# Kernel tuning notes

Measured on AMD Instinct MI355X. Metric: run time of the kernel, lower is better.

The kernel has to match this reference:

```python
import jax, jax.numpy as jnp
import numpy as np

EPS = 1e-5

def rmsnorm(x, g):
    var = jnp.mean(jnp.square(x), axis=-1, keepdims=True)
    return x * jax.lax.rsqrt(var + EPS) * g

def setup_inputs() -> dict:
    key = jax.random.key(0)
    ks = jax.random.split(key, 8)
    B, S, T, D = 2, 2048, 2048, 1024
    H, HKV, HD = 16, 4, 64
    std = 0.02
    return {
        "x": jax.random.normal(ks[0], (B, S, D), jnp.float32),
        "kv": jax.random.normal(ks[1], (B, T, D), jnp.float32),
        "wq": jax.random.normal(ks[2], (H * HD, D), jnp.float32) * std,
        "wk": jax.random.normal(ks[3], (HKV * HD, D), jnp.float32) * std,
        "wv": jax.random.normal(ks[4], (HKV * HD, D), jnp.float32) * std,
        "wo": jax.random.normal(ks[5], (D, H * HD), jnp.float32) * std,
        "gq": jnp.ones((D,), jnp.float32),
        "gkv": jnp.ones((D,), jnp.float32),
    }

def reference(x, kv, wq, wk, wv, wo, gq, gkv):
    B, S, D = x.shape
    T = kv.shape[1]
    H, HKV, HD = 16, 4, 64
    R = H // HKV  # heads per kv group
    xn = rmsnorm(x, gq)
    kvn = rmsnorm(kv, gkv)
    # projections
    q = (xn @ wq.T).reshape(B, S, HKV, R, HD)   # grouped query heads
    k = (kvn @ wk.T).reshape(B, T, HKV, HD)
    v = (kvn @ wv.T).reshape(B, T, HKV, HD)
    scale = 1.0 / jnp.sqrt(jnp.float32(HD))
    # block-mask is None -> full dense cross attention; GQA via broadcast einsum
    scores = jnp.einsum('bsgrd,btgd->bgrst', q, k) * scale  # [B,HKV,R,S,T]
    probs = jax.nn.softmax(scores, axis=-1)
    out = jnp.einsum('bgrst,btgd->bsgrd', probs, v)  # [B,S,HKV,R,HD]
    out = out.reshape(B, S, H * HD) @ wo.T
    return x + out
```

## Files before the change

### kernel.cpp

```cpp
#include <hip/hip_runtime.h>

#define DEV __device__ __forceinline__

typedef __attribute__((ext_vector_type(8))) _Float16 h8;
typedef __attribute__((ext_vector_type(4))) float f32x4;
typedef __attribute__((ext_vector_type(16))) float f32x16;
typedef __fp16 __attribute__((ext_vector_type(2))) hh2;

DEV unsigned short f2h(float f) {
  union { _Float16 h[2]; unsigned short u[2]; } v;
  v.h[0] = (_Float16)f;
  return v.u[0];
}

DEV float h2f(unsigned short u) {
  union { _Float16 h[2]; unsigned short u[2]; } v;
  v.u[0] = u;
  return (float)v.h[0];
}

DEV void async_load16(const void* g, void* l) {
  __builtin_amdgcn_global_load_lds(
      (const __attribute__((address_space(1))) void*)g,
      (__attribute__((address_space(3))) void*)l,
      16, 0, 0);
}

DEV void pl32swap(unsigned int& a, unsigned int& b) {
  asm("v_permlane32_swap_b32 %0, %1" : "+v"(a), "+v"(b));
}


__global__ __launch_bounds__(256) void prep(const float* __restrict__ x,
                                            const float* __restrict__ kv,
                                            const float* __restrict__ wq,
                                            const float* __restrict__ wk,
                                            const float* __restrict__ wv,
                                            const float* __restrict__ wo,
                                            const float* __restrict__ gq,
                                            const float* __restrict__ gkv,
                                            unsigned short* __restrict__ wqb,
                                            unsigned short* __restrict__ wkvb,
                                            unsigned short* __restrict__ wob,
                                            unsigned short* __restrict__ xn,
                                            unsigned short* __restrict__ kvn,
                                            float qscale) {
  const int b = blockIdx.x, tid = threadIdx.x;
  if (b < 2560) {
    const float* src;
    unsigned short* dst;
    float sc = 1.0f;
    int base;
    if (b < 1024) { src = wq; dst = wqb; sc = qscale; base = b; }
    else if (b < 1280) { src = wk; dst = wkvb; base = b - 1024; }
    else if (b < 1536) { src = wv; dst = wkvb + 262144; base = b - 1280; }
    else { src = wo; dst = wob; base = b - 1536; }
    const int i = (base * 256 + tid) * 4;
    float4 v = *(const float4*)&src[i];
    ushort4 o;
    o.x = f2h(v.x * sc); o.y = f2h(v.y * sc);
    o.z = f2h(v.z * sc); o.w = f2h(v.w * sc);
    *(ushort4*)&dst[i] = o;
    return;
  }
  int row = b - 2560;
  const float* src;
  const float* g;
  unsigned short* dst;
  if (row < 4096) { src = x; g = gq; dst = xn; }
  else { row -= 4096; src = kv; g = gkv; dst = kvn; }
  const float* xr = src + (size_t)row * 1024;
  float4 v = *(const float4*)&xr[tid * 4];
  float ss = v.x * v.x + v.y * v.y + v.z * v.z + v.w * v.w;
  ss += __shfl_xor(ss, 32); ss += __shfl_xor(ss, 16);
  ss += __shfl_xor(ss, 8);  ss += __shfl_xor(ss, 4);
  ss += __shfl_xor(ss, 2);  ss += __shfl_xor(ss, 1);
  __shared__ float red[4];
  if ((tid & 63) == 0) red[tid >> 6] = ss;
  __syncthreads();
  float tot = red[0] + red[1] + red[2] + red[3];
  float inv = rsqrtf(tot * (1.0f / 1024.0f) + 1e-5f);
  float4 gv = *(const float4*)&g[tid * 4];
  ushort4 o;
  o.x = f2h(v.x * inv * gv.x); o.y = f2h(v.y * inv * gv.y);
  o.z = f2h(v.z * inv * gv.z); o.w = f2h(v.w * inv * gv.w);
  *(ushort4*)&dst[(size_t)row * 1024 + tid * 4] = o;
}

__global__ __launch_bounds__(256) void proj_gemm(const unsigned short* __restrict__ xn,
                                                 const unsigned short* __restrict__ kvn,
                                                 const unsigned short* __restrict__ wqb,
                                                 const unsigned short* __restrict__ wkvb,
                                                 unsigned short* __restrict__ qb,
                                                 unsigned short* __restrict__ kb,
                                                 unsigned short* __restrict__ vTb) {
  __shared__ unsigned short Al[2][2][128 * 32];
  __shared__ unsigned short Bl[2][2][64 * 32];
  const int tid = threadIdx.x;
  const int w = tid >> 6, l = tid & 63;
  const int quad = l >> 4, ln = l & 15;
  const int wm0 = (w >> 1) * 64, wn0 = (w & 1) * 32;
  const int r4 = l >> 2;
  const int c4s = (((l & 3) ^ ((l >> 3) & 3))) * 8;
  const int qs8 = (quad ^ ((l >> 1) & 3)) * 8;

  int z = blockIdx.x;
  const unsigned short *A, *W;
  int m0, n0, isq;
  if (z < 512) {
    A = xn; W = wqb; isq = 1;
    m0 = (((z >> 7) << 3) + (z & 7)) * 128;
    n0 = ((z >> 3) & 15) * 64;
  } else {
    z -= 512; A = kvn; W = wkvb; isq = 0;
    m0 = (((z >> 6) << 3) + (z & 7)) * 128;
    n0 = ((z >> 3) & 7) * 64;
  }

  f32x4 acc[4][2] = {};

  auto stage = [&](int buf, int kk) {
#pragma unroll
    for (int j = 0; j < 6; ++j) {
      const int idx = w * 6 + j;
      if (idx < 16) {
        const int p = idx >> 3, rb = (idx & 7) * 16;
        async_load16(A + (size_t)(m0 + rb + r4) * 1024 + kk + p * 32 + c4s,
                     &Al[buf][p][rb * 32]);
      } else {
        const int ib = idx - 16;
        const int p = ib >> 2, rb = (ib & 3) * 16;
        async_load16(W + (size_t)(n0 + rb + r4) * 1024 + kk + p * 32 + c4s,
                     &Bl[buf][p][rb * 32]);
      }
    }
  };

  stage(0, 0);
#pragma unroll 2
  for (int it = 0; it < 16; ++it) {
    const int buf = it & 1;
    __syncthreads();
    if (it < 15) stage(buf ^ 1, (it + 1) * 64);
#pragma unroll
    for (int kc = 0; kc < 2; ++kc) {
      h8 af[4], bf[2];
#pragma unroll
      for (int mi = 0; mi < 4; ++mi)
        af[mi] = *(const h8*)&Al[buf][kc][(wm0 + mi * 16 + ln) * 32 + qs8];
#pragma unroll
      for (int ni = 0; ni < 2; ++ni)
        bf[ni] = *(const h8*)&Bl[buf][kc][(wn0 + ni * 16 + ln) * 32 + qs8];
#pragma unroll
      for (int mi = 0; mi < 4; ++mi)
#pragma unroll
        for (int ni = 0; ni < 2; ++ni)
          acc[mi][ni] = __builtin_amdgcn_mfma_f32_16x16x32_f16(af[mi], bf[ni], acc[mi][ni], 0, 0, 0);
    }
  }

#pragma unroll
  for (int mi = 0; mi < 4; ++mi)
#pragma unroll
    for (int ni = 0; ni < 2; ++ni)
#pragma unroll
      for (int r = 0; r < 4; ++r) {
        const int row = m0 + wm0 + mi * 16 + quad * 4 + r;
        const int col = n0 + wn0 + ni * 16 + ln;
        const unsigned short v = f2h(acc[mi][ni][r]);
        if (isq) {
          qb[((size_t)row << 10) + col] = v;
        } else if (col < 256) {
          kb[(size_t)row * 256 + col] = v;
        } else {
          const int c2 = col - 256, gg = c2 >> 6, dd = c2 & 63;
          const int bb = row >> 11, t = row & 2047;
          vTb[((size_t)((bb * 4 + gg) * 64 + dd) << 11) + t] = v;
        }
      }
}

__global__ __launch_bounds__(256) void o_gemm(const unsigned short* __restrict__ O0,
                                              const unsigned short* __restrict__ O1,
                                              const float* __restrict__ l0p,
                                              const float* __restrict__ l1p,
                                              const unsigned short* __restrict__ wob,
                                              const float* __restrict__ x,
                                              float* __restrict__ out) {
  __shared__ unsigned short Al[2][2][128 * 32];
  __shared__ unsigned short Bl[2][2][64 * 32];
  __shared__ float Linv[16 * 128];
  const int tid = threadIdx.x;
  const int w = tid >> 6, l = tid & 63;
  const int quad = l >> 4, ln = l & 15;
  const int wm0 = (w >> 1) * 64, wn0 = (w & 1) * 32;
  const int r4 = l >> 2;
  const int c4s = (((l & 3) ^ ((l >> 3) & 3))) * 8;
  const int qs8 = (quad ^ ((l >> 1) & 3)) * 8;

  const int z = blockIdx.x;
  const int m0 = (((z >> 7) << 3) + (z & 7)) * 128;
  const int n0 = ((z >> 3) & 15) * 64;

  {
    const int h = tid >> 4, r0 = (tid & 15) * 8;
#pragma unroll
    for (int i = 0; i < 8; ++i) {
      const int r = r0 + i;
      const size_t li = (size_t)(m0 + r) * 16 + h;
      Linv[h * 128 + r] = 1.0f / (l0p[li] + l1p[li]);
    }
  }
  __syncthreads();

  const int srow = tid >> 3;
  const int sp = (tid >> 2) & 1;
  const int ss = tid & 3;

  auto stageA = [&](int buf, int kk) {
    const int h = kk >> 6;
#pragma unroll
    for (int ps = 0; ps < 4; ++ps) {
      const int row = ps * 32 + srow;
      const size_t gidx = (size_t)(m0 + row) * 1024 + kk + sp * 32 + ss * 8;
      h8 a0 = *(const h8*)&O0[gidx];
      h8 a1 = *(const h8*)&O1[gidx];
      const _Float16 lv = (_Float16)Linv[h * 128 + row];
      h8 sum = a0 + a1;
#pragma unroll
      for (int q2 = 0; q2 < 8; ++q2) sum[q2] *= lv;
      const int sl = ss ^ ((row >> 1) & 3);
      *(h8*)&Al[buf][sp][row * 32 + sl * 8] = sum;
    }
  };
  auto stageB = [&](int buf, int kk) {
#pragma unroll
    for (int j = 0; j < 2; ++j) {
      const int ib = w * 2 + j;
      const int p = ib >> 2, rb = (ib & 3) * 16;
      async_load16(wob + (size_t)(n0 + rb + r4) * 1024 + kk + p * 32 + c4s,
                   &Bl[buf][p][rb * 32]);
    }
  };

  f32x4 acc[4][2] = {};
  stageB(0, 0);
  stageA(0, 0);
  for (int it = 0; it < 16; ++it) {
    const int buf = it & 1;
    __syncthreads();
    if (it < 15) { stageB(buf ^ 1, (it + 1) * 64); stageA(buf ^ 1, (it + 1) * 64); }
#pragma unroll
    for (int kc = 0; kc < 2; ++kc) {
      h8 af[4], bf[2];
#pragma unroll
      for (int mi = 0; mi < 4; ++mi)
        af[mi] = *(const h8*)&Al[buf][kc][(wm0 + mi * 16 + ln) * 32 + qs8];
#pragma unroll
      for (int ni = 0; ni < 2; ++ni)
        bf[ni] = *(const h8*)&Bl[buf][kc][(wn0 + ni * 16 + ln) * 32 + qs8];
#pragma unroll
      for (int mi = 0; mi < 4; ++mi)
#pragma unroll
        for (int ni = 0; ni < 2; ++ni)
          acc[mi][ni] = __builtin_amdgcn_mfma_f32_16x16x32_f16(af[mi], bf[ni], acc[mi][ni], 0, 0, 0);
    }
  }

#pragma unroll
  for (int mi = 0; mi < 4; ++mi)
#pragma unroll
    for (int ni = 0; ni < 2; ++ni)
#pragma unroll
      for (int r = 0; r < 4; ++r) {
        const int row = m0 + wm0 + mi * 16 + quad * 4 + r;
        const int col = n0 + wn0 + ni * 16 + ln;
        const size_t idx = ((size_t)row << 10) + col;
        out[idx] = x[idx] + acc[mi][ni][r];
      }
}

__global__ __launch_bounds__(256, 4) void flash_attn(const unsigned short* __restrict__ q,
                                                     const unsigned short* __restrict__ k,
                                                     const unsigned short* __restrict__ vT,
                                                     unsigned short* __restrict__ o0,
                                                     unsigned short* __restrict__ o1,
                                                     float* __restrict__ l0p,
                                                     float* __restrict__ l1p) {
  __shared__ unsigned short Kl[2][64 * 64];
  __shared__ unsigned short Vl[2][64 * 64];

  const int tid = threadIdx.x;
  const int w = tid >> 6, l = tid & 63;
  const int lq = l & 31, hi = l >> 5;
  const int r8 = l >> 3, c8 = l & 7;
  const int csw = (c8 ^ r8) * 8;
  const int s0 = blockIdx.x * 128;
  const int h = blockIdx.y, g = h >> 2;
  const int b = blockIdx.z >> 1, ts = blockIdx.z & 1;
  const int tbase = ts << 10;

  unsigned short* Opart = ts ? o1 : o0;
  float* lpart = ts ? l1p : l0p;

  const size_t qrow = (size_t)(b * 2048 + s0 + w * 32 + lq);

  h8 qf[4];
#pragma unroll
  for (int ks = 0; ks < 4; ++ks)
    qf[ks] = *(const h8*)&q[(qrow << 10) + h * 64 + ks * 16 + hi * 8];

  f32x16 oaccT[2] = {};
  float lsum = 0.0f;

  const unsigned short* kbase = k + ((size_t)(b * 2048)) * 256 + g * 64;
  const unsigned short* vbase = vT + (((size_t)(b * 4 + g) * 64) << 11);

  const hh2 one2 = {(__fp16)1.0f, (__fp16)1.0f};

  auto stage = [&](int buf, int t0) {
#pragma unroll
    for (int j = 0; j < 2; ++j) {
      const int idx = w * 2 + j;
      async_load16(kbase + (size_t)(t0 + idx * 8 + r8) * 256 + csw,
                   &Kl[buf][idx * 512]);
      async_load16(vbase + (((size_t)(idx * 8 + r8)) << 11) + t0 + csw,
                   &Vl[buf][idx * 512]);
    }
  };

  stage(0, tbase);
  for (int it = 0; it < 16; ++it) {
    const int buf = it & 1;
    __syncthreads();
    if (it < 15) stage(buf ^ 1, tbase + (it + 1) * 64);

#pragma unroll
    for (int tblk = 0; tblk < 2; ++tblk) {
      f32x16 st = {};
      __builtin_amdgcn_s_setprio(1);
#pragma unroll
      for (int ks = 0; ks < 4; ++ks) {
        const int t = tblk * 32 + lq;
        h8 kf = *(const h8*)&Kl[buf][t * 64 + ((2 * ks + hi) ^ (t & 7)) * 8];
        st = __builtin_amdgcn_mfma_f32_32x32x16_f16(kf, qf[ks], st, 0, 0, 0);
      }
      __builtin_amdgcn_s_setprio(0);

      unsigned int wj[8];
#pragma unroll
      for (int j = 0; j < 8; ++j) {
        const float p0 = __builtin_amdgcn_exp2f(st[2 * j]);
        const float p1 = __builtin_amdgcn_exp2f(st[2 * j + 1]);
        union { hh2 h2; unsigned int u; } pk;
        pk.h2 = __builtin_amdgcn_cvt_pkrtz(p0, p1);
        wj[j] = pk.u;
#if __has_builtin(__builtin_amdgcn_fdot2)
        lsum = __builtin_amdgcn_fdot2(pk.h2, one2, lsum, false);
#else
        lsum += p0 + p1;
#endif
      }

      unsigned int a0 = wj[0], b0 = wj[2]; pl32swap(a0, b0);
      unsigned int a1 = wj[1], b1 = wj[3]; pl32swap(a1, b1);
      unsigned int a4 = wj[4], b4 = wj[6]; pl32swap(a4, b4);
      unsigned int a5 = wj[5], b5 = wj[7]; pl32swap(a5, b5);
      union { unsigned int u[4]; h8 v; } f0, f1;
      f0.u[0] = a0; f0.u[1] = a1; f0.u[2] = b0; f0.u[3] = b1;
      f1.u[0] = a4; f1.u[1] = a5; f1.u[2] = b4; f1.u[3] = b5;

      __builtin_amdgcn_s_setprio(1);
#pragma unroll
      for (int dblk = 0; dblk < 2; ++dblk) {
        const int d = dblk * 32 + lq;
        h8 v0 = *(const h8*)&Vl[buf][d * 64 + ((2 * (2 * tblk + 0) + hi) ^ (d & 7)) * 8];
        oaccT[dblk] = __builtin_amdgcn_mfma_f32_32x32x16_f16(v0, f0.v, oaccT[dblk], 0, 0, 0);
        h8 v1 = *(const h8*)&Vl[buf][d * 64 + ((2 * (2 * tblk + 1) + hi) ^ (d & 7)) * 8];
        oaccT[dblk] = __builtin_amdgcn_mfma_f32_32x32x16_f16(v1, f1.v, oaccT[dblk], 0, 0, 0);
      }
      __builtin_amdgcn_s_setprio(0);
    }
  }

  lsum += __shfl_xor(lsum, 32);
  if (l < 32) lpart[qrow * 16 + h] = lsum;

#pragma unroll
  for (int dblk = 0; dblk < 2; ++dblk)
#pragma unroll
    for (int qd = 0; qd < 4; ++qd) {
      ushort4 o;
      o.x = f2h(oaccT[dblk][qd * 4 + 0]);
      o.y = f2h(oaccT[dblk][qd * 4 + 1]);
      o.z = f2h(oaccT[dblk][qd * 4 + 2]);
      o.w = f2h(oaccT[dblk][qd * 4 + 3]);
      *(ushort4*)&Opart[(qrow << 10) + h * 64 + dblk * 32 + qd * 8 + hi * 4] = o;
    }
}

extern "C" void kernel_launch(void* const* d_in, const int* in_sizes, int n_in,
                              void* d_out, int out_size, void* d_ws, size_t ws_size,
                              hipStream_t stream) {
  const float* x   = (const float*)d_in[0];
  const float* kv  = (const float*)d_in[1];
  const float* wq  = (const float*)d_in[2];
  const float* wk  = (const float*)d_in[3];
  const float* wv  = (const float*)d_in[4];
  const float* wo  = (const float*)d_in[5];
  const float* gq  = (const float*)d_in[6];
  const float* gkv = (const float*)d_in[7];

  char* ws = (char*)d_ws;
  unsigned short* xn   = (unsigned short*)(ws);
  unsigned short* kvn  = (unsigned short*)(ws + 8388608);
  unsigned short* qb   = (unsigned short*)(ws + 16777216);
  unsigned short* kb   = (unsigned short*)(ws + 25165824);
  unsigned short* vTb  = (unsigned short*)(ws + 27262976);
  unsigned short* wqb  = (unsigned short*)(ws + 37748736);
  unsigned short* wkvb = (unsigned short*)(ws + 39845888);
  unsigned short* wob  = (unsigned short*)(ws + 40894464);
  unsigned short* Opart0 = xn;
  unsigned short* Opart1 = kvn;
  float* l0p = (float*)wqb;
  float* l1p = (float*)(ws + 37748736 + 262144);

  const float qscale = 0.18033688011112042f;

  prep<<<10752, 256, 0, stream>>>(x, kv, wq, wk, wv, wo, gq, gkv,
                                  wqb, wkvb, wob, xn, kvn, qscale);

  proj_gemm<<<768, 256, 0, stream>>>(xn, kvn, wqb, wkvb, qb, kb, vTb);

  flash_attn<<<dim3(16, 16, 4), 256, 0, stream>>>(qb, kb, vTb, Opart0, Opart1, l0p, l1p);

  o_gemm<<<512, 256, 0, stream>>>(Opart0, Opart1, l0p, l1p, wob, x, (float*)d_out);
}
```

Measured before the change: 195.7 us.

## Triple-buffer K/V tiles in flash attention with vmcnt-based barriers and interleaved MFMAs

Changes the flash attention K/V staging from double to triple buffering, so two tiles are in flight while a third is computed. The per-iteration __syncthreads is replaced by an explicit s_waitcnt vmcnt plus s_barrier. The loop is manually unrolled by three, LDS offsets are precomputed, and the two 32-row score blocks are computed together so their MFMAs, exps and row sums interleave. The extra LDS buffer and the extra live registers lower the occupancy hint from 4 to 3 blocks, trading occupancy for deeper prefetch and more instruction-level parallelism.

```diff
diff --git a/kernel.cpp b/kernel.cpp
--- a/kernel.cpp
+++ b/kernel.cpp
@@ -280,21 +280,22 @@
       }
 }
 
-__global__ __launch_bounds__(256, 4) void flash_attn(const unsigned short* __restrict__ q,
+__global__ __launch_bounds__(256, 3) void flash_attn(const unsigned short* __restrict__ q,
                                                      const unsigned short* __restrict__ k,
                                                      const unsigned short* __restrict__ vT,
                                                      unsigned short* __restrict__ o0,
                                                      unsigned short* __restrict__ o1,
                                                      float* __restrict__ l0p,
                                                      float* __restrict__ l1p) {
-  __shared__ unsigned short Kl[2][64 * 64];
-  __shared__ unsigned short Vl[2][64 * 64];
+  __shared__ __align__(16) unsigned short Kl[3][64 * 64];
+  __shared__ __align__(16) unsigned short Vl[3][64 * 64];
 
   const int tid = threadIdx.x;
   const int w = tid >> 6, l = tid & 63;
   const int lq = l & 31, hi = l >> 5;
   const int r8 = l >> 3, c8 = l & 7;
   const int csw = (c8 ^ r8) * 8;
+  const int rsw = lq & 7;
   const int s0 = blockIdx.x * 128;
   const int h = blockIdx.y, g = h >> 2;
   const int b = blockIdx.z >> 1, ts = blockIdx.z & 1;
@@ -309,80 +310,118 @@
 #pragma unroll
   for (int ks = 0; ks < 4; ++ks)
     qf[ks] = *(const h8*)&q[(qrow << 10) + h * 64 + ks * 16 + hi * 8];
-
-  f32x16 oaccT[2] = {};
-  float lsum = 0.0f;
+  asm volatile("s_waitcnt vmcnt(0)" ::: "memory");
+
+  int aoff[4];
+#pragma unroll
+  for (int j = 0; j < 4; ++j)
+    aoff[j] = (lq * 64 + (((2 * j + hi) ^ rsw)) * 8) * 2;
+
+  f32x16 oacc[2] = {};
+  float lsA = 0.0f, lsB = 0.0f;
 
   const unsigned short* kbase = k + ((size_t)(b * 2048)) * 256 + g * 64;
   const unsigned short* vbase = vT + (((size_t)(b * 4 + g) * 64) << 11);
 
   const hh2 one2 = {(__fp16)1.0f, (__fp16)1.0f};
 
-  auto stage = [&](int buf, int t0) {
+  auto stage = [&](int sb, int t0) {
 #pragma unroll
     for (int j = 0; j < 2; ++j) {
       const int idx = w * 2 + j;
       async_load16(kbase + (size_t)(t0 + idx * 8 + r8) * 256 + csw,
-                   &Kl[buf][idx * 512]);
+                   &Kl[sb][idx * 512]);
       async_load16(vbase + (((size_t)(idx * 8 + r8)) << 11) + t0 + csw,
-                   &Vl[buf][idx * 512]);
+                   &Vl[sb][idx * 512]);
     }
   };
 
+#define FA_SYNC(N)                                                   \
+  do {                                                               \
+    asm volatile("s_waitcnt vmcnt(" #N ")" ::: "memory");            \
+    __builtin_amdgcn_s_barrier();                                    \
+    __builtin_amdgcn_sched_barrier(0);                               \
+  } while (0)
+
+#define FA_BODY(CB)                                                            \
+  {                                                                            \
+    h8 kf0[4], kf1[4];                                                         \
+    _Pragma("unroll")                                                          \
+    for (int ks = 0; ks < 4; ++ks) {                                           \
+      kf0[ks] = *(const h8*)((const char*)&Kl[CB][0] + aoff[ks]);              \
+      kf1[ks] = *(const h8*)((const char*)&Kl[CB][2048] + aoff[ks]);           \
+    }                                                                          \
+    f32x16 st0 = {}, st1 = {};                                                 \
+    __builtin_amdgcn_s_setprio(1);                                             \
+    _Pragma("unroll")                                                          \
+    for (int ks = 0; ks < 4; ++ks) {                                           \
+      st0 = __builtin_amdgcn_mfma_f32_32x32x16_f16(kf0[ks], qf[ks], st0, 0, 0, 0); \
+      st1 = __builtin_amdgcn_mfma_f32_32x32x16_f16(kf1[ks], qf[ks], st1, 0, 0, 0); \
+    }                                                                          \
+    __builtin_amdgcn_s_setprio(0);                                             \
+    unsigned int w0_[8], w1_[8];                                               \
+    _Pragma("unroll")                                                          \
+    for (int j = 0; j < 8; ++j) {                                              \
+      union { hh2 h2; unsigned int u; } pk0, pk1;                              \
+      pk0.h2 = __builtin_amdgcn_cvt_pkrtz(__builtin_amdgcn_exp2f(st0[2 * j]),  \
+                                          __builtin_amdgcn_exp2f(st0[2 * j + 1])); \
+      pk1.h2 = __builtin_amdgcn_cvt_pkrtz(__builtin_amdgcn_exp2f(st1[2 * j]),  \
+                                          __builtin_amdgcn_exp2f(st1[2 * j + 1])); \
+      lsA = __builtin_amdgcn_fdot2(pk0.h2, one2, lsA, false);                  \
+      lsB = __builtin_amdgcn_fdot2(pk1.h2, one2, lsB, false);                  \
+      w0_[j] = pk0.u; w1_[j] = pk1.u;                                          \
+    }                                                                          \
+    h8 pf[4];                                                                  \
+    {                                                                          \
+      unsigned int a0 = w0_[0], b0 = w0_[2]; pl32swap(a0, b0);                 \
+      unsigned int a1 = w0_[1], b1 = w0_[3]; pl32swap(a1, b1);                 \
+      unsigned int a4 = w0_[4], b4 = w0_[6]; pl32swap(a4, b4);                 \
+      unsigned int a5 = w0_[5], b5 = w0_[7]; pl32swap(a5, b5);                 \
+      union { unsigned int u[4]; h8 v; } f0, f1;                               \
+      f0.u[0] = a0; f0.u[1] = a1; f0.u[2] = b0; f0.u[3] = b1;                  \
+      f1.u[0] = a4; f1.u[1] = a5; f1.u[2] = b4; f1.u[3] = b5;                  \
+      pf[0] = f0.v; pf[1] = f1.v;                                              \
+      unsigned int c0 = w1_[0], d0 = w1_[2]; pl32swap(c0, d0);                 \
+      unsigned int c1 = w1_[1], d1 = w1_[3]; pl32swap(c1, d1);                 \
+      unsigned int c4 = w1_[4], d4 = w1_[6]; pl32swap(c4, d4);                 \
+      unsigned int c5 = w1_[5], d5 = w1_[7]; pl32swap(c5, d5);                 \
+      union { unsigned int u[4]; h8 v; } f2, f3;                               \
+      f2.u[0] = c0; f2.u[1] = c1; f2.u[2] = d0; f2.u[3] = d1;                  \
+      f3.u[0] = c4; f3.u[1] = c5; f3.u[2] = d4; f3.u[3] = d5;                  \
+      pf[2] = f2.v; pf[3] = f3.v;                                              \
+    }                                                                          \
+    __builtin_amdgcn_s_setprio(1);                                             \
+    _Pragma("unroll")                                                          \
+    for (int c = 0; c < 4; ++c) {                                              \
+      h8 v0 = *(const h8*)((const char*)&Vl[CB][0] + aoff[c]);                 \
+      h8 v1 = *(const h8*)((const char*)&Vl[CB][2048] + aoff[c]);              \
+      oacc[0] = __builtin_amdgcn_mfma_f32_32x32x16_f16(v0, pf[c], oacc[0], 0, 0, 0); \
+      oacc[1] = __builtin_amdgcn_mfma_f32_32x32x16_f16(v1, pf[c], oacc[1], 0, 0, 0); \
+    }                                                                          \
+    __builtin_amdgcn_s_setprio(0);                                             \
+  }
+
   stage(0, tbase);
-  for (int it = 0; it < 16; ++it) {
-    const int buf = it & 1;
-    __syncthreads();
-    if (it < 15) stage(buf ^ 1, tbase + (it + 1) * 64);
-
-#pragma unroll
-    for (int tblk = 0; tblk < 2; ++tblk) {
-      f32x16 st = {};
-      __builtin_amdgcn_s_setprio(1);
-#pragma unroll
-      for (int ks = 0; ks < 4; ++ks) {
-        const int t = tblk * 32 + lq;
-        h8 kf = *(const h8*)&Kl[buf][t * 64 + ((2 * ks + hi) ^ (t & 7)) * 8];
-        st = __builtin_amdgcn_mfma_f32_32x32x16_f16(kf, qf[ks], st, 0, 0, 0);
-      }
-      __builtin_amdgcn_s_setprio(0);
-
-      unsigned int wj[8];
-#pragma unroll
-      for (int j = 0; j < 8; ++j) {
-        const float p0 = __builtin_amdgcn_exp2f(st[2 * j]);
-        const float p1 = __builtin_amdgcn_exp2f(st[2 * j + 1]);
-        union { hh2 h2; unsigned int u; } pk;
-        pk.h2 = __builtin_amdgcn_cvt_pkrtz(p0, p1);
-        wj[j] = pk.u;
-#if __has_builtin(__builtin_amdgcn_fdot2)
-        lsum = __builtin_amdgcn_fdot2(pk.h2, one2, lsum, false);
-#else
-        lsum += p0 + p1;
-#endif
-      }
-
-      unsigned int a0 = wj[0], b0 = wj[2]; pl32swap(a0, b0);
-      unsigned int a1 = wj[1], b1 = wj[3]; pl32swap(a1, b1);
-      unsigned int a4 = wj[4], b4 = wj[6]; pl32swap(a4, b4);
-      unsigned int a5 = wj[5], b5 = wj[7]; pl32swap(a5, b5);
-      union { unsigned int u[4]; h8 v; } f0, f1;
-      f0.u[0] = a0; f0.u[1] = a1; f0.u[2] = b0; f0.u[3] = b1;
-      f1.u[0] = a4; f1.u[1] = a5; f1.u[2] = b4; f1.u[3] = b5;
-
-      __builtin_amdgcn_s_setprio(1);
-#pragma unroll
-      for (int dblk = 0; dblk < 2; ++dblk) {
-        const int d = dblk * 32 + lq;
-        h8 v0 = *(const h8*)&Vl[buf][d * 64 + ((2 * (2 * tblk + 0) + hi) ^ (d & 7)) * 8];
-        oaccT[dblk] = __builtin_amdgcn_mfma_f32_32x32x16_f16(v0, f0.v, oaccT[dblk], 0, 0, 0);
-        h8 v1 = *(const h8*)&Vl[buf][d * 64 + ((2 * (2 * tblk + 1) + hi) ^ (d & 7)) * 8];
-        oaccT[dblk] = __builtin_amdgcn_mfma_f32_32x32x16_f16(v1, f1.v, oaccT[dblk], 0, 0, 0);
-      }
-      __builtin_amdgcn_s_setprio(0);
-    }
-  }
-
+  stage(1, tbase + 64);
+
+  for (int tt = 0; tt < 15; tt += 3) {
+    FA_SYNC(4);
+    stage(2, tbase + (tt + 2) * 64);
+    FA_BODY(0);
+    FA_SYNC(4);
+    stage(0, tbase + (tt + 3) * 64);
+    FA_BODY(1);
+    FA_SYNC(4);
+    if (tt + 4 < 16) stage(1, tbase + (tt + 4) * 64);
+    FA_BODY(2);
+  }
+  FA_SYNC(0);
+  FA_BODY(0);
+
+#undef FA_BODY
+#undef FA_SYNC
+
+  float lsum = lsA + lsB;
   lsum += __shfl_xor(lsum, 32);
   if (l < 32) lpart[qrow * 16 + h] = lsum;
 
@@ -391,10 +430,10 @@
 #pragma unroll
     for (int qd = 0; qd < 4; ++qd) {
       ushort4 o;
-      o.x = f2h(oaccT[dblk][qd * 4 + 0]);
-      o.y = f2h(oaccT[dblk][qd * 4 + 1]);
-      o.z = f2h(oaccT[dblk][qd * 4 + 2]);
-      o.w = f2h(oaccT[dblk][qd * 4 + 3]);
+      o.x = f2h(oacc[dblk][qd * 4 + 0]);
+      o.y = f2h(oacc[dblk][qd * 4 + 1]);
+      o.z = f2h(oacc[dblk][qd * 4 + 2]);
+      o.w = f2h(oacc[dblk][qd * 4 + 3]);
       *(ushort4*)&Opart[(qrow << 10) + h * 64 + dblk * 32 + qd * 8 + hi * 4] = o;
     }
 }
```

Result: no change. 194.4 us (-0.6%).
